# Performance work log

Measured on AMD Instinct MI355X. Metric: run time of the kernel, lower is better.

## Reference

```python
import jax, jax.numpy as jnp
import numpy as np

N = 50000
E = 800000
NEG_SLOPE = 0.2


def gat_layer(x, src, dst, W, al, ar):
    # x: [N, F_in]; W: [F_in, H*D]; al/ar: [H, D]
    H, D = al.shape
    feat = (x @ W).reshape(N, H, D)                      # [N, H, D]
    el = jnp.einsum('nhd,hd->nh', feat, al)              # [N, H]
    er = jnp.einsum('nhd,hd->nh', feat, ar)              # [N, H]
    e = jax.nn.leaky_relu(el[src] + er[dst], NEG_SLOPE)  # [E, H]
    # segment softmax over edges grouped by destination node
    m = jax.ops.segment_max(e, dst, num_segments=N)      # [N, H] (-inf for empty)
    a = jnp.exp(e - m[dst])                              # [E, H]
    s = jax.ops.segment_sum(a, dst, num_segments=N)      # [N, H]
    a = a / jnp.where(s[dst] > 0, s[dst], 1.0)
    # weighted gather-aggregate of messages
    out = jax.ops.segment_sum(a[:, :, None] * feat[src], dst, num_segments=N)
    return out                                           # [N, H, D]


def setup_inputs() -> dict:
    key = jax.random.key(0)
    ks = jax.random.split(key, 9)
    in_size, hid, out_size = 512, 64, 64
    H1, H2 = 4, 4
    return {
        'x':   jax.random.normal(ks[0], (N, in_size), dtype=jnp.float32),
        'src': jax.random.randint(ks[1], (E,), 0, N, dtype=jnp.int32),
        'dst': jax.random.randint(ks[2], (E,), 0, N, dtype=jnp.int32),
        'W1':  jax.random.normal(ks[3], (in_size, H1 * hid), dtype=jnp.float32) * 0.05,
        'al1': jax.random.normal(ks[4], (H1, hid), dtype=jnp.float32) * 0.1,
        'ar1': jax.random.normal(ks[5], (H1, hid), dtype=jnp.float32) * 0.1,
        'W2':  jax.random.normal(ks[6], (H1 * hid, H2 * out_size), dtype=jnp.float32) * 0.05,
        'al2': jax.random.normal(ks[7], (H2, out_size), dtype=jnp.float32) * 0.1,
        'ar2': jax.random.normal(ks[8], (H2, out_size), dtype=jnp.float32) * 0.1,
    }


def reference(x, src, dst, W1, al1, ar1, W2, al2, ar2):
    h = gat_layer(x, src, dst, W1, al1, ar1)   # [N, H1, hid]
    h = jax.nn.elu(h).reshape(N, -1)           # flatten heads -> [N, H1*hid]
    h = gat_layer(h, src, dst, W2, al2, ar2)   # [N, H2, out]
    return h.mean(axis=1)                      # mean over heads -> [N, out]
```

## Files before the change

kernel.cpp:

```cpp
#include <hip/hip_runtime.h>

#define NNODES 50000
#define NEDGES 800000
#define HH 4
#define DD 64
#define FEAT 256
#define NB ((NNODES + 255) / 256)
#define MPAD 50048

typedef __attribute__((ext_vector_type(8))) _Float16 frag16;
typedef __attribute__((ext_vector_type(4))) float frag_cd;
typedef __attribute__((ext_vector_type(4))) _Float16 h4v;
typedef __attribute__((ext_vector_type(8))) _Float16 h8v;

__global__ __launch_bounds__(256) void prep_w_kernel(
    const float* __restrict__ W1, const float* __restrict__ W2,
    _Float16* __restrict__ Bp1, _Float16* __restrict__ Bp2) {
  int idx = blockIdx.x * 256 + threadIdx.x;
  if (idx < 512 * 256) {
    int k = idx >> 8, n = idx & 255;
    Bp1[(size_t)n * 512 + k] = (_Float16)W1[idx];
  } else {
    idx -= 512 * 256;
    int k = idx >> 8, n = idx & 255;
    Bp2[(size_t)n * 256 + k] = (_Float16)W2[idx];
  }
}

template <int AF32>
__global__ __launch_bounds__(512) void mfma_gemm_kernel(
    const void* __restrict__ Av, const _Float16* __restrict__ Bp,
    _Float16* __restrict__ featb, const float* __restrict__ al,
    const float* __restrict__ ar, float* __restrict__ elp,
    float* __restrict__ erp, int M, int K) {
  __shared__ _Float16 As[128 * 64];
  __shared__ _Float16 Bs[256 * 64];
  const int tid = threadIdx.x;
  const int w = tid >> 6, lane = tid & 63;
  const int q = lane >> 4, ln = lane & 15;
  const int rowBase = blockIdx.x * 128;
  const int wm = (w >> 2) * 64;
  const int wn = (w & 3) * 64;

  frag_cd acc[4][4] = {};

  const int i1 = K >> 6;
  const int srow8 = lane >> 3;
  const int scg = ((lane & 7) ^ srow8) * 8;
  const int sw = ln & 7;

  const int ar_ = tid >> 2, aq = tid & 3;
  const int as0 = ((aq * 2) ^ (ar_ & 7)) * 8;
  const int as1 = ((aq * 2 + 1) ^ (ar_ & 7)) * 8;

  for (int it = 0; it < i1; ++it) {
    const int kk = it << 6;
    __syncthreads();
    if constexpr (AF32) {
      const float* __restrict__ x = (const float*)Av;
      float4 v0, v1, v2, v3;
      v0 = v1 = v2 = v3 = make_float4(0.f, 0.f, 0.f, 0.f);
      int xrow = rowBase + ar_;
      if (xrow < M) {
        const float4* xp = (const float4*)(x + (size_t)xrow * 512 + kk + aq * 16);
        v0 = xp[0]; v1 = xp[1]; v2 = xp[2]; v3 = xp[3];
      }
      frag16 f0, f1;
      f0[0] = (_Float16)v0.x; f0[1] = (_Float16)v0.y;
      f0[2] = (_Float16)v0.z; f0[3] = (_Float16)v0.w;
      f0[4] = (_Float16)v1.x; f0[5] = (_Float16)v1.y;
      f0[6] = (_Float16)v1.z; f0[7] = (_Float16)v1.w;
      f1[0] = (_Float16)v2.x; f1[1] = (_Float16)v2.y;
      f1[2] = (_Float16)v2.z; f1[3] = (_Float16)v2.w;
      f1[4] = (_Float16)v3.x; f1[5] = (_Float16)v3.y;
      f1[6] = (_Float16)v3.z; f1[7] = (_Float16)v3.w;
      *(frag16*)&As[ar_ * 64 + as0] = f0;
      *(frag16*)&As[ar_ * 64 + as1] = f1;
    } else {
      const _Float16* __restrict__ Ap = (const _Float16*)Av;
#pragma unroll
      for (int j = 0; j < 2; ++j) {
        int rloc = w * 16 + j * 8 + srow8;
        __builtin_amdgcn_global_load_lds(
            (const __attribute__((address_space(1))) void*)(Ap + (size_t)(rowBase + rloc) * K + kk + scg),
            (__attribute__((address_space(3))) void*)(&As[(w * 16 + j * 8) * 64 + lane * 8]), 16, 0, 0);
      }
    }
#pragma unroll
    for (int j = 0; j < 4; ++j) {
      int rloc = w * 32 + j * 8 + srow8;
      __builtin_amdgcn_global_load_lds(
          (const __attribute__((address_space(1))) void*)(Bp + (size_t)rloc * K + kk + scg),
          (__attribute__((address_space(3))) void*)(&Bs[(w * 32 + j * 8) * 64 + lane * 8]), 16, 0, 0);
    }
    __syncthreads();

#pragma unroll
    for (int ksub = 0; ksub < 2; ++ksub) {
      const int slot = ((ksub * 4 + q) ^ sw) * 8;
      frag16 a[4], b[4];
#pragma unroll
      for (int i = 0; i < 4; ++i)
        a[i] = *(const frag16*)&As[(wm + i * 16 + ln) * 64 + slot];
#pragma unroll
      for (int j = 0; j < 4; ++j)
        b[j] = *(const frag16*)&Bs[(wn + j * 16 + ln) * 64 + slot];
#pragma unroll
      for (int i = 0; i < 4; ++i)
#pragma unroll
        for (int j = 0; j < 4; ++j)
          acc[i][j] = __builtin_amdgcn_mfma_f32_16x16x32_f16(a[i], b[j], acc[i][j], 0, 0, 0);
    }
  }

#pragma unroll
  for (int i = 0; i < 4; ++i) {
    int rowg = rowBase + wm + i * 16 + q * 4;
#pragma unroll
    for (int r = 0; r < 4; ++r) {
      int row = rowg + r;
      if (row < M) {
#pragma unroll
        for (int j = 0; j < 4; ++j) {
          int col = wn + j * 16 + ln;
          featb[(size_t)row * 256 + col] = (_Float16)acc[i][j][r];
        }
      }
    }
  }

  const int h = wn >> 6;
  float alv[4], arv[4];
#pragma unroll
  for (int j = 0; j < 4; ++j) {
    alv[j] = al[h * DD + j * 16 + ln];
    arv[j] = ar[h * DD + j * 16 + ln];
  }
#pragma unroll
  for (int i = 0; i < 4; ++i) {
#pragma unroll
    for (int r = 0; r < 4; ++r) {
      float pl = 0.f, pr = 0.f;
#pragma unroll
      for (int j = 0; j < 4; ++j) {
        pl = fmaf(acc[i][j][r], alv[j], pl);
        pr = fmaf(acc[i][j][r], arv[j], pr);
      }
#pragma unroll
      for (int msk = 1; msk < 16; msk <<= 1) {
        pl += __shfl_xor(pl, msk);
        pr += __shfl_xor(pr, msk);
      }
      int row = rowBase + wm + i * 16 + q * 4 + r;
      if (ln == 0 && row < M) {
        elp[row * HH + h] = pl;
        erp[row * HH + h] = pr;
      }
    }
  }
}

__global__ __launch_bounds__(256) void hist_kernel(const int* __restrict__ dst,
                                                   int* __restrict__ deg) {
  int e = blockIdx.x * 256 + threadIdx.x;
  if (e < NEDGES) atomicAdd(&deg[dst[e]], 1);
}

__global__ __launch_bounds__(256) void scan_block_kernel(const int* __restrict__ deg,
                                                         int* __restrict__ off,
                                                         int* __restrict__ bsum) {
  __shared__ int tmp[256];
  int b = blockIdx.x, t = threadIdx.x;
  int i = b * 256 + t;
  int v = (i < NNODES) ? deg[i] : 0;
  tmp[t] = v;
  __syncthreads();
  for (int s = 1; s < 256; s <<= 1) {
    int add = (t >= s) ? tmp[t - s] : 0;
    __syncthreads();
    tmp[t] += add;
    __syncthreads();
  }
  if (i < NNODES) off[i + 1] = tmp[t];
  if (t == 255) bsum[b] = tmp[255];
}

__global__ __launch_bounds__(256) void scan_top_kernel(int* __restrict__ bsum) {
  __shared__ int tmp[256];
  int t = threadIdx.x;
  int v = (t < NB) ? bsum[t] : 0;
  tmp[t] = v;
  __syncthreads();
  for (int s = 1; s < 256; s <<= 1) {
    int add = (t >= s) ? tmp[t - s] : 0;
    __syncthreads();
    tmp[t] += add;
    __syncthreads();
  }
  if (t < NB) bsum[t] = tmp[t] - v;
}

__global__ __launch_bounds__(256) void scan_add_kernel(int* __restrict__ off,
                                                       const int* __restrict__ bsum,
                                                       int* __restrict__ cursor) {
  int b = blockIdx.x, t = threadIdx.x;
  int i = b * 256 + t;
  if (i < NNODES) {
    int val = off[i + 1] + bsum[b];
    off[i + 1] = val;
    if (i + 1 < NNODES) cursor[i + 1] = val;
  }
  if (i == 0) { off[0] = 0; cursor[0] = 0; }
}

__global__ __launch_bounds__(256) void scatter_kernel(const int* __restrict__ src,
                                                      const int* __restrict__ dst,
                                                      int* __restrict__ cursor,
                                                      int* __restrict__ csr_src) {
  int e = blockIdx.x * 256 + threadIdx.x;
  if (e >= NEDGES) return;
  int d = dst[e];
  int pos = atomicAdd(&cursor[d], 1);
  csr_src[pos] = src[e];
}

template <int LAYER>
__global__ __launch_bounds__(256) void gat_agg_kernel(
    const int* __restrict__ off, const int* __restrict__ csr_src,
    const float* __restrict__ el, const float* __restrict__ er,
    const _Float16* __restrict__ featb, float* __restrict__ outp,
    _Float16* __restrict__ outs) {
  __shared__ float sA[4][HH][68];
  __shared__ int sS[4][64];
  const int w = threadIdx.x >> 6;
  const int lane = threadIdx.x & 63;
  const int n = blockIdx.x * 4 + w;
  const int beg = off[n];
  const int deg = off[n + 1] - beg;

  const int half = lane >> 5;
  const int fl = lane & 31;
  const int fb = fl << 3;
  const int hh = fl >> 3;

  float acc[8] = {0.f, 0.f, 0.f, 0.f, 0.f, 0.f, 0.f, 0.f};

  if (deg > 0 && deg <= 64) {
    const int h1 = lane & 3, j1 = lane >> 2;
    const float erd = er[n * HH + h1];
    float e[4], a[4];
    float m = -INFINITY;
#pragma unroll
    for (int p = 0; p < 4; ++p) {
      int j = j1 + p * 16;
      int s = 0;
      float ev = -INFINITY;
      if (j < deg) {
        s = csr_src[beg + j];
        ev = el[s * HH + h1] + erd;
        ev = ev > 0.f ? ev : 0.2f * ev;
      }
      if (h1 == 0) sS[w][j] = s;
      e[p] = ev;
      m = fmaxf(m, ev);
    }
#pragma unroll
    for (int msk = 4; msk <= 32; msk <<= 1) m = fmaxf(m, __shfl_xor(m, msk));
    float ps = 0.f;
#pragma unroll
    for (int p = 0; p < 4; ++p) {
      a[p] = (j1 + p * 16 < deg) ? __expf(e[p] - m) : 0.f;
      ps += a[p];
    }
#pragma unroll
    for (int msk = 4; msk <= 32; msk <<= 1) ps += __shfl_xor(ps, msk);
    const float sinv = 1.f / ps;
#pragma unroll
    for (int p = 0; p < 4; ++p) {
      int j = j1 + p * 16;
      sA[w][h1][j] = a[p] * sinv;
    }

    const int deg2 = (deg + 1) & ~1;
    int j = 0;
    for (; j + 8 <= deg2; j += 8) {
      int s0 = sS[w][j + half];
      int s1 = sS[w][j + 2 + half];
      int s2 = sS[w][j + 4 + half];
      int s3 = sS[w][j + 6 + half];
      float a0 = sA[w][hh][j + half];
      float a1 = sA[w][hh][j + 2 + half];
      float a2 = sA[w][hh][j + 4 + half];
      float a3 = sA[w][hh][j + 6 + half];
      h8v u0 = *(const h8v*)&featb[(size_t)s0 * FEAT + fb];
      h8v u1 = *(const h8v*)&featb[(size_t)s1 * FEAT + fb];
      h8v u2 = *(const h8v*)&featb[(size_t)s2 * FEAT + fb];
      h8v u3 = *(const h8v*)&featb[(size_t)s3 * FEAT + fb];
#pragma unroll
      for (int c = 0; c < 8; ++c) acc[c] = fmaf(a0, (float)u0[c], acc[c]);
#pragma unroll
      for (int c = 0; c < 8; ++c) acc[c] = fmaf(a1, (float)u1[c], acc[c]);
#pragma unroll
      for (int c = 0; c < 8; ++c) acc[c] = fmaf(a2, (float)u2[c], acc[c]);
#pragma unroll
      for (int c = 0; c < 8; ++c) acc[c] = fmaf(a3, (float)u3[c], acc[c]);
    }
    for (; j < deg2; j += 2) {
      int s0 = sS[w][j + half];
      float a0 = sA[w][hh][j + half];
      h8v u0 = *(const h8v*)&featb[(size_t)s0 * FEAT + fb];
#pragma unroll
      for (int c = 0; c < 8; ++c) acc[c] = fmaf(a0, (float)u0[c], acc[c]);
    }
  } else if (deg > 64) {
    const int h1 = lane & 3, j1 = lane >> 2;
    const float erd = er[n * HH + h1];
    float m = -INFINITY;
    for (int j = j1; j < deg; j += 16) {
      int s = csr_src[beg + j];
      float ev = el[s * HH + h1] + erd;
      ev = ev > 0.f ? ev : 0.2f * ev;
      m = fmaxf(m, ev);
    }
#pragma unroll
    for (int msk = 4; msk <= 32; msk <<= 1) m = fmaxf(m, __shfl_xor(m, msk));
    float ps = 0.f;
    for (int j = j1; j < deg; j += 16) {
      int s = csr_src[beg + j];
      float ev = el[s * HH + h1] + erd;
      ev = ev > 0.f ? ev : 0.2f * ev;
      ps += __expf(ev - m);
    }
#pragma unroll
    for (int msk = 4; msk <= 32; msk <<= 1) ps += __shfl_xor(ps, msk);
    const float m2 = __shfl(m, hh);
    const float psinv2 = 1.f / __shfl(ps, hh);
    const float erd2 = er[n * HH + hh];
    for (int j = half; j < deg; j += 2) {
      int s = csr_src[beg + j];
      float ev = el[s * HH + hh] + erd2;
      ev = ev > 0.f ? ev : 0.2f * ev;
      float a0 = __expf(ev - m2) * psinv2;
      h8v u0 = *(const h8v*)&featb[(size_t)s * FEAT + fb];
#pragma unroll
      for (int c = 0; c < 8; ++c) acc[c] = fmaf(a0, (float)u0[c], acc[c]);
    }
  }

#pragma unroll
  for (int c = 0; c < 8; ++c) acc[c] += __shfl_xor(acc[c], 32);

  if (LAYER == 1) {
    if (half == 0) {
      h8v o;
#pragma unroll
      for (int c = 0; c < 8; ++c) {
        float v = acc[c];
        v = v > 0.f ? v : (__expf(v) - 1.f);
        o[c] = (_Float16)v;
      }
      *(h8v*)&outs[(size_t)n * 256 + fb] = o;
    }
  } else {
#pragma unroll
    for (int c = 0; c < 8; ++c) {
      acc[c] += __shfl_xor(acc[c], 8);
      acc[c] += __shfl_xor(acc[c], 16);
    }
    if (lane < 8) {
      float4 o1 = make_float4(0.25f * acc[0], 0.25f * acc[1],
                              0.25f * acc[2], 0.25f * acc[3]);
      float4 o2 = make_float4(0.25f * acc[4], 0.25f * acc[5],
                              0.25f * acc[6], 0.25f * acc[7]);
      *(float4*)&outp[(size_t)n * DD + (lane << 3)] = o1;
      *(float4*)&outp[(size_t)n * DD + (lane << 3) + 4] = o2;
    }
  }
}

extern "C" void kernel_launch(void* const* d_in, const int* in_sizes, int n_in,
                              void* d_out, int out_size, void* d_ws, size_t ws_size,
                              hipStream_t stream) {
  const float* x   = (const float*)d_in[0];
  const int*   src = (const int*)d_in[1];
  const int*   dst = (const int*)d_in[2];
  const float* W1  = (const float*)d_in[3];
  const float* al1 = (const float*)d_in[4];
  const float* ar1 = (const float*)d_in[5];
  const float* W2  = (const float*)d_in[6];
  const float* al2 = (const float*)d_in[7];
  const float* ar2 = (const float*)d_in[8];
  float* out = (float*)d_out;

  float* ws = (float*)d_ws;
  float* el = ws;
  float* er = el + NNODES * HH;
  int* deg     = (int*)(er + NNODES * HH);
  int* off     = deg + NNODES;
  int* cursor  = off + NNODES + 1;
  int* bsum    = cursor + NNODES;
  int* csr_src = bsum + 256;
  uintptr_t p = ((uintptr_t)(csr_src + NEDGES) + 63) & ~(uintptr_t)63;
  _Float16* featb = (_Float16*)p;
  _Float16* Apr = featb + (size_t)NNODES * 256;
  Apr = (_Float16*)(((uintptr_t)Apr + 63) & ~(uintptr_t)63);
  _Float16* Bpr1 = Apr + (size_t)MPAD * 256;
  _Float16* Bpr2 = Bpr1 + 256 * 512;

  const int edgeBlocks = (NEDGES + 255) / 256;

  hipMemsetAsync(deg, 0, NNODES * sizeof(int), stream);
  hist_kernel<<<edgeBlocks, 256, 0, stream>>>(dst, deg);
  scan_block_kernel<<<NB, 256, 0, stream>>>(deg, off, bsum);
  scan_top_kernel<<<1, 256, 0, stream>>>(bsum);
  scan_add_kernel<<<NB, 256, 0, stream>>>(off, bsum, cursor);
  scatter_kernel<<<edgeBlocks, 256, 0, stream>>>(src, dst, cursor, csr_src);

  prep_w_kernel<<<768, 256, 0, stream>>>(W1, W2, Bpr1, Bpr2);

  mfma_gemm_kernel<1><<<MPAD / 128, 512, 0, stream>>>(x, Bpr1, featb, al1, ar1, el, er, NNODES, 512);
  gat_agg_kernel<1><<<NNODES / 4, 256, 0, stream>>>(off, csr_src, el, er, featb, nullptr, Apr);

  mfma_gemm_kernel<0><<<MPAD / 128, 512, 0, stream>>>(Apr, Bpr2, featb, al2, ar2, el, er, NNODES, 256);
  gat_agg_kernel<2><<<NNODES / 4, 256, 0, stream>>>(off, csr_src, el, er, featb, out, nullptr);
}
```

Baseline: 409.7 us.

## Double-buffer GEMM with smaller M tile, fuse histogram/weight prep, single-block scan

The GEMM tile shrinks from 128 to 64 rows, so twice as many blocks launch, and shared-memory staging becomes double-buffered so the next K slice loads while MFMAs run on the current one. The histogram and weight-transpose kernels merge into one launch. The three-kernel prefix scan becomes a single 1024-thread block that scans 49 elements per thread serially. Together these cut launch count and hide GEMM load latency, at the cost of more B-tile reloads per row and a serial, strided scan pass.

```diff
diff --git a/kernel.cpp b/kernel.cpp
--- a/kernel.cpp
+++ b/kernel.cpp
@@ -5,212 +5,64 @@
 #define HH 4
 #define DD 64
 #define FEAT 256
-#define NB ((NNODES + 255) / 256)
 #define MPAD 50048
+#define EDGEBLOCKS ((NEDGES + 255) / 256)
 
 typedef __attribute__((ext_vector_type(8))) _Float16 frag16;
 typedef __attribute__((ext_vector_type(4))) float frag_cd;
 typedef __attribute__((ext_vector_type(4))) _Float16 h4v;
 typedef __attribute__((ext_vector_type(8))) _Float16 h8v;
 
-__global__ __launch_bounds__(256) void prep_w_kernel(
+__global__ __launch_bounds__(256) void front_kernel(
+    const int* __restrict__ dst, int* __restrict__ deg,
     const float* __restrict__ W1, const float* __restrict__ W2,
     _Float16* __restrict__ Bp1, _Float16* __restrict__ Bp2) {
-  int idx = blockIdx.x * 256 + threadIdx.x;
-  if (idx < 512 * 256) {
-    int k = idx >> 8, n = idx & 255;
-    Bp1[(size_t)n * 512 + k] = (_Float16)W1[idx];
+  int b = blockIdx.x;
+  if (b < EDGEBLOCKS) {
+    int e = b * 256 + threadIdx.x;
+    if (e < NEDGES) atomicAdd(&deg[dst[e]], 1);
   } else {
-    idx -= 512 * 256;
-    int k = idx >> 8, n = idx & 255;
-    Bp2[(size_t)n * 256 + k] = (_Float16)W2[idx];
-  }
-}
-
-template <int AF32>
-__global__ __launch_bounds__(512) void mfma_gemm_kernel(
-    const void* __restrict__ Av, const _Float16* __restrict__ Bp,
-    _Float16* __restrict__ featb, const float* __restrict__ al,
-    const float* __restrict__ ar, float* __restrict__ elp,
-    float* __restrict__ erp, int M, int K) {
-  __shared__ _Float16 As[128 * 64];
-  __shared__ _Float16 Bs[256 * 64];
-  const int tid = threadIdx.x;
-  const int w = tid >> 6, lane = tid & 63;
-  const int q = lane >> 4, ln = lane & 15;
-  const int rowBase = blockIdx.x * 128;
-  const int wm = (w >> 2) * 64;
-  const int wn = (w & 3) * 64;
-
-  frag_cd acc[4][4] = {};
-
-  const int i1 = K >> 6;
-  const int srow8 = lane >> 3;
-  const int scg = ((lane & 7) ^ srow8) * 8;
-  const int sw = ln & 7;
-
-  const int ar_ = tid >> 2, aq = tid & 3;
-  const int as0 = ((aq * 2) ^ (ar_ & 7)) * 8;
-  const int as1 = ((aq * 2 + 1) ^ (ar_ & 7)) * 8;
-
-  for (int it = 0; it < i1; ++it) {
-    const int kk = it << 6;
+    int idx = (b - EDGEBLOCKS) * 256 + threadIdx.x;
+    if (idx < 512 * 256) {
+      int k = idx >> 8, n = idx & 255;
+      Bp1[(size_t)n * 512 + k] = (_Float16)W1[idx];
+    } else {
+      idx -= 512 * 256;
+      int k = idx >> 8, n = idx & 255;
+      Bp2[(size_t)n * 256 + k] = (_Float16)W2[idx];
+    }
+  }
+}
+
+__global__ __launch_bounds__(1024) void scan_kernel(const int* __restrict__ deg,
+                                                    int* __restrict__ off,
+                                                    int* __restrict__ cursor) {
+  __shared__ int part[1024];
+  const int t = threadIdx.x;
+  const int b0 = t * 49;
+  int s = 0;
+  for (int k = 0; k < 49; ++k) {
+    int i = b0 + k;
+    s += (i < NNODES) ? deg[i] : 0;
+  }
+  part[t] = s;
+  __syncthreads();
+  for (int st = 1; st < 1024; st <<= 1) {
+    int add = (t >= st) ? part[t - st] : 0;
     __syncthreads();
-    if constexpr (AF32) {
-      const float* __restrict__ x = (const float*)Av;
-      float4 v0, v1, v2, v3;
-      v0 = v1 = v2 = v3 = make_float4(0.f, 0.f, 0.f, 0.f);
-      int xrow = rowBase + ar_;
-      if (xrow < M) {
-        const float4* xp = (const float4*)(x + (size_t)xrow * 512 + kk + aq * 16);
-        v0 = xp[0]; v1 = xp[1]; v2 = xp[2]; v3 = xp[3];
-      }
-      frag16 f0, f1;
-      f0[0] = (_Float16)v0.x; f0[1] = (_Float16)v0.y;
-      f0[2] = (_Float16)v0.z; f0[3] = (_Float16)v0.w;
-      f0[4] = (_Float16)v1.x; f0[5] = (_Float16)v1.y;
-      f0[6] = (_Float16)v1.z; f0[7] = (_Float16)v1.w;
-      f1[0] = (_Float16)v2.x; f1[1] = (_Float16)v2.y;
-      f1[2] = (_Float16)v2.z; f1[3] = (_Float16)v2.w;
-      f1[4] = (_Float16)v3.x; f1[5] = (_Float16)v3.y;
-      f1[6] = (_Float16)v3.z; f1[7] = (_Float16)v3.w;
-      *(frag16*)&As[ar_ * 64 + as0] = f0;
-      *(frag16*)&As[ar_ * 64 + as1] = f1;
-    } else {
-      const _Float16* __restrict__ Ap = (const _Float16*)Av;
-#pragma unroll
-      for (int j = 0; j < 2; ++j) {
-        int rloc = w * 16 + j * 8 + srow8;
-        __builtin_amdgcn_global_load_lds(
-            (const __attribute__((address_space(1))) void*)(Ap + (size_t)(rowBase + rloc) * K + kk + scg),
-            (__attribute__((address_space(3))) void*)(&As[(w * 16 + j * 8) * 64 + lane * 8]), 16, 0, 0);
-      }
-    }
-#pragma unroll
-    for (int j = 0; j < 4; ++j) {
-      int rloc = w * 32 + j * 8 + srow8;
-      __builtin_amdgcn_global_load_lds(
-          (const __attribute__((address_space(1))) void*)(Bp + (size_t)rloc * K + kk + scg),
-          (__attribute__((address_space(3))) void*)(&Bs[(w * 32 + j * 8) * 64 + lane * 8]), 16, 0, 0);
-    }
+    part[t] += add;
     __syncthreads();
-
-#pragma unroll
-    for (int ksub = 0; ksub < 2; ++ksub) {
-      const int slot = ((ksub * 4 + q) ^ sw) * 8;
-      frag16 a[4], b[4];
-#pragma unroll
-      for (int i = 0; i < 4; ++i)
-        a[i] = *(const frag16*)&As[(wm + i * 16 + ln) * 64 + slot];
-#pragma unroll
-      for (int j = 0; j < 4; ++j)
-        b[j] = *(const frag16*)&Bs[(wn + j * 16 + ln) * 64 + slot];
-#pragma unroll
-      for (int i = 0; i < 4; ++i)
-#pragma unroll
-        for (int j = 0; j < 4; ++j)
-          acc[i][j] = __builtin_amdgcn_mfma_f32_16x16x32_f16(a[i], b[j], acc[i][j], 0, 0, 0);
-    }
-  }
-
-#pragma unroll
-  for (int i = 0; i < 4; ++i) {
-    int rowg = rowBase + wm + i * 16 + q * 4;
-#pragma unroll
-    for (int r = 0; r < 4; ++r) {
-      int row = rowg + r;
-      if (row < M) {
-#pragma unroll
-        for (int j = 0; j < 4; ++j) {
-          int col = wn + j * 16 + ln;
-          featb[(size_t)row * 256 + col] = (_Float16)acc[i][j][r];
-        }
-      }
-    }
-  }
-
-  const int h = wn >> 6;
-  float alv[4], arv[4];
-#pragma unroll
-  for (int j = 0; j < 4; ++j) {
-    alv[j] = al[h * DD + j * 16 + ln];
-    arv[j] = ar[h * DD + j * 16 + ln];
-  }
-#pragma unroll
-  for (int i = 0; i < 4; ++i) {
-#pragma unroll
-    for (int r = 0; r < 4; ++r) {
-      float pl = 0.f, pr = 0.f;
-#pragma unroll
-      for (int j = 0; j < 4; ++j) {
-        pl = fmaf(acc[i][j][r], alv[j], pl);
-        pr = fmaf(acc[i][j][r], arv[j], pr);
-      }
-#pragma unroll
-      for (int msk = 1; msk < 16; msk <<= 1) {
-        pl += __shfl_xor(pl, msk);
-        pr += __shfl_xor(pr, msk);
-      }
-      int row = rowBase + wm + i * 16 + q * 4 + r;
-      if (ln == 0 && row < M) {
-        elp[row * HH + h] = pl;
-        erp[row * HH + h] = pr;
-      }
-    }
-  }
-}
-
-__global__ __launch_bounds__(256) void hist_kernel(const int* __restrict__ dst,
-                                                   int* __restrict__ deg) {
-  int e = blockIdx.x * 256 + threadIdx.x;
-  if (e < NEDGES) atomicAdd(&deg[dst[e]], 1);
-}
-
-__global__ __launch_bounds__(256) void scan_block_kernel(const int* __restrict__ deg,
-                                                         int* __restrict__ off,
-                                                         int* __restrict__ bsum) {
-  __shared__ int tmp[256];
-  int b = blockIdx.x, t = threadIdx.x;
-  int i = b * 256 + t;
-  int v = (i < NNODES) ? deg[i] : 0;
-  tmp[t] = v;
-  __syncthreads();
-  for (int s = 1; s < 256; s <<= 1) {
-    int add = (t >= s) ? tmp[t - s] : 0;
-    __syncthreads();
-    tmp[t] += add;
-    __syncthreads();
-  }
-  if (i < NNODES) off[i + 1] = tmp[t];
-  if (t == 255) bsum[b] = tmp[255];
-}
-
-__global__ __launch_bounds__(256) void scan_top_kernel(int* __restrict__ bsum) {
-  __shared__ int tmp[256];
-  int t = threadIdx.x;
-  int v = (t < NB) ? bsum[t] : 0;
-  tmp[t] = v;
-  __syncthreads();
-  for (int s = 1; s < 256; s <<= 1) {
-    int add = (t >= s) ? tmp[t - s] : 0;
-    __syncthreads();
-    tmp[t] += add;
-    __syncthreads();
-  }
-  if (t < NB) bsum[t] = tmp[t] - v;
-}
-
-__global__ __launch_bounds__(256) void scan_add_kernel(int* __restrict__ off,
-                                                       const int* __restrict__ bsum,
-                                                       int* __restrict__ cursor) {
-  int b = blockIdx.x, t = threadIdx.x;
-  int i = b * 256 + t;
-  if (i < NNODES) {
-    int val = off[i + 1] + bsum[b];
-    off[i + 1] = val;
-    if (i + 1 < NNODES) cursor[i + 1] = val;
-  }
-  if (i == 0) { off[0] = 0; cursor[0] = 0; }
+  }
+  int run = (t == 0) ? 0 : part[t - 1];
+  for (int k = 0; k < 49; ++k) {
+    int i = b0 + k;
+    if (i < NNODES) {
+      off[i] = run;
+      cursor[i] = run;
+      run += deg[i];
+    }
+  }
+  if (t == 1023) off[NNODES] = part[1023];
 }
 
 __global__ __launch_bounds__(256) void scatter_kernel(const int* __restrict__ src,
@@ -222,6 +74,169 @@
   int d = dst[e];
   int pos = atomicAdd(&cursor[d], 1);
   csr_src[pos] = src[e];
+}
+
+template <int AF32>
+__global__ __launch_bounds__(512) void mfma_gemm_kernel(
+    const void* __restrict__ Av, const _Float16* __restrict__ Bp,
+    _Float16* __restrict__ featb, const float* __restrict__ al,
+    const float* __restrict__ ar, float* __restrict__ elp,
+    float* __restrict__ erp, int M, int K) {
+  __shared__ _Float16 As[2][64 * 64];
+  __shared__ _Float16 Bs[2][256 * 64];
+  const int tid = threadIdx.x;
+  const int w = tid >> 6, lane = tid & 63;
+  const int q = lane >> 4, ln = lane & 15;
+  const int rowBase = blockIdx.x * 64;
+  const int wm = (w >> 2) * 32;
+  const int wn = (w & 3) * 64;
+
+  frag_cd acc[2][4] = {};
+
+  const int nt = K >> 6;
+  const int srow8 = lane >> 3;
+  const int scg = ((lane & 7) ^ srow8) * 8;
+  const int sw = ln & 7;
+
+  const int ar_ = tid >> 3, ao = tid & 7;
+  const int aslot = (ao ^ (ar_ & 7)) * 8;
+  const int xrow = rowBase + ar_;
+
+  const float* __restrict__ x = (const float*)Av;
+  const _Float16* __restrict__ Ap = (const _Float16*)Av;
+
+  float4 av0, av1;
+
+  {
+    const int kk = 0;
+    if constexpr (AF32) {
+      av0 = av1 = make_float4(0.f, 0.f, 0.f, 0.f);
+      if (xrow < M) {
+        const float4* xp = (const float4*)(x + (size_t)xrow * 512 + kk + ao * 8);
+        av0 = xp[0]; av1 = xp[1];
+      }
+    } else {
+      __builtin_amdgcn_global_load_lds(
+          (const __attribute__((address_space(1))) void*)(Ap + (size_t)(rowBase + w * 8 + srow8) * K + kk + scg),
+          (__attribute__((address_space(3))) void*)(&As[0][(w * 8) * 64 + lane * 8]), 16, 0, 0);
+    }
+#pragma unroll
+    for (int j = 0; j < 4; ++j) {
+      int rloc = w * 32 + j * 8 + srow8;
+      __builtin_amdgcn_global_load_lds(
+          (const __attribute__((address_space(1))) void*)(Bp + (size_t)rloc * K + kk + scg),
+          (__attribute__((address_space(3))) void*)(&Bs[0][(w * 32 + j * 8) * 64 + lane * 8]), 16, 0, 0);
+    }
+    if constexpr (AF32) {
+      frag16 f;
+      f[0] = (_Float16)av0.x; f[1] = (_Float16)av0.y;
+      f[2] = (_Float16)av0.z; f[3] = (_Float16)av0.w;
+      f[4] = (_Float16)av1.x; f[5] = (_Float16)av1.y;
+      f[6] = (_Float16)av1.z; f[7] = (_Float16)av1.w;
+      *(frag16*)&As[0][ar_ * 64 + aslot] = f;
+    }
+  }
+
+  for (int t = 0; t < nt; ++t) {
+    const int cur = t & 1, nxt = cur ^ 1;
+    __syncthreads();
+
+    if (t + 1 < nt) {
+      const int kk = (t + 1) << 6;
+      if constexpr (AF32) {
+        av0 = av1 = make_float4(0.f, 0.f, 0.f, 0.f);
+        if (xrow < M) {
+          const float4* xp = (const float4*)(x + (size_t)xrow * 512 + kk + ao * 8);
+          av0 = xp[0]; av1 = xp[1];
+        }
+      } else {
+        __builtin_amdgcn_global_load_lds(
+            (const __attribute__((address_space(1))) void*)(Ap + (size_t)(rowBase + w * 8 + srow8) * K + kk + scg),
+            (__attribute__((address_space(3))) void*)(&As[nxt][(w * 8) * 64 + lane * 8]), 16, 0, 0);
+      }
+#pragma unroll
+      for (int j = 0; j < 4; ++j) {
+        int rloc = w * 32 + j * 8 + srow8;
+        __builtin_amdgcn_global_load_lds(
+            (const __attribute__((address_space(1))) void*)(Bp + (size_t)rloc * K + kk + scg),
+            (__attribute__((address_space(3))) void*)(&Bs[nxt][(w * 32 + j * 8) * 64 + lane * 8]), 16, 0, 0);
+      }
+    }
+
+#pragma unroll
+    for (int ksub = 0; ksub < 2; ++ksub) {
+      const int slot = ((ksub * 4 + q) ^ sw) * 8;
+      frag16 a[2], b[4];
+#pragma unroll
+      for (int i = 0; i < 2; ++i)
+        a[i] = *(const frag16*)&As[cur][(wm + i * 16 + ln) * 64 + slot];
+#pragma unroll
+      for (int j = 0; j < 4; ++j)
+        b[j] = *(const frag16*)&Bs[cur][(wn + j * 16 + ln) * 64 + slot];
+#pragma unroll
+      for (int i = 0; i < 2; ++i)
+#pragma unroll
+        for (int j = 0; j < 4; ++j)
+          acc[i][j] = __builtin_amdgcn_mfma_f32_16x16x32_f16(a[i], b[j], acc[i][j], 0, 0, 0);
+    }
+
+    if constexpr (AF32) {
+      if (t + 1 < nt) {
+        frag16 f;
+        f[0] = (_Float16)av0.x; f[1] = (_Float16)av0.y;
+        f[2] = (_Float16)av0.z; f[3] = (_Float16)av0.w;
+        f[4] = (_Float16)av1.x; f[5] = (_Float16)av1.y;
+        f[6] = (_Float16)av1.z; f[7] = (_Float16)av1.w;
+        *(frag16*)&As[nxt][ar_ * 64 + aslot] = f;
+      }
+    }
+  }
+
+#pragma unroll
+  for (int i = 0; i < 2; ++i) {
+    int rowg = rowBase + wm + i * 16 + q * 4;
+#pragma unroll
+    for (int r = 0; r < 4; ++r) {
+      int row = rowg + r;
+      if (row < M) {
+#pragma unroll
+        for (int j = 0; j < 4; ++j) {
+          int col = wn + j * 16 + ln;
+          featb[(size_t)row * 256 + col] = (_Float16)acc[i][j][r];
+        }
+      }
+    }
+  }
+
+  const int h = wn >> 6;
+  float alv[4], arv[4];
+#pragma unroll
+  for (int j = 0; j < 4; ++j) {
+    alv[j] = al[h * DD + j * 16 + ln];
+    arv[j] = ar[h * DD + j * 16 + ln];
+  }
+#pragma unroll
+  for (int i = 0; i < 2; ++i) {
+#pragma unroll
+    for (int r = 0; r < 4; ++r) {
+      float pl = 0.f, pr = 0.f;
+#pragma unroll
+      for (int j = 0; j < 4; ++j) {
+        pl = fmaf(acc[i][j][r], alv[j], pl);
+        pr = fmaf(acc[i][j][r], arv[j], pr);
+      }
+#pragma unroll
+      for (int msk = 1; msk < 16; msk <<= 1) {
+        pl += __shfl_xor(pl, msk);
+        pr += __shfl_xor(pr, msk);
+      }
+      int row = rowBase + wm + i * 16 + q * 4 + r;
+      if (ln == 0 && row < M) {
+        elp[row * HH + h] = pl;
+        erp[row * HH + h] = pr;
+      }
+    }
+  }
 }
 
 template <int LAYER>
@@ -398,8 +413,7 @@
   int* deg     = (int*)(er + NNODES * HH);
   int* off     = deg + NNODES;
   int* cursor  = off + NNODES + 1;
-  int* bsum    = cursor + NNODES;
-  int* csr_src = bsum + 256;
+  int* csr_src = cursor + NNODES;
   uintptr_t p = ((uintptr_t)(csr_src + NEDGES) + 63) & ~(uintptr_t)63;
   _Float16* featb = (_Float16*)p;
   _Float16* Apr = featb + (size_t)NNODES * 256;
@@ -407,20 +421,14 @@
   _Float16* Bpr1 = Apr + (size_t)MPAD * 256;
   _Float16* Bpr2 = Bpr1 + 256 * 512;
 
-  const int edgeBlocks = (NEDGES + 255) / 256;
-
   hipMemsetAsync(deg, 0, NNODES * sizeof(int), stream);
-  hist_kernel<<<edgeBlocks, 256, 0, stream>>>(dst, deg);
-  scan_block_kernel<<<NB, 256, 0, stream>>>(deg, off, bsum);
-  scan_top_kernel<<<1, 256, 0, stream>>>(bsum);
-  scan_add_kernel<<<NB, 256, 0, stream>>>(off, bsum, cursor);
-  scatter_kernel<<<edgeBlocks, 256, 0, stream>>>(src, dst, cursor, csr_src);
-
-  prep_w_kernel<<<768, 256, 0, stream>>>(W1, W2, Bpr1, Bpr2);
-
-  mfma_gemm_kernel<1><<<MPAD / 128, 512, 0, stream>>>(x, Bpr1, featb, al1, ar1, el, er, NNODES, 512);
+  front_kernel<<<EDGEBLOCKS + 768, 256, 0, stream>>>(dst, deg, W1, W2, Bpr1, Bpr2);
+  scan_kernel<<<1, 1024, 0, stream>>>(deg, off, cursor);
+  scatter_kernel<<<EDGEBLOCKS, 256, 0, stream>>>(src, dst, cursor, csr_src);
+
+  mfma_gemm_kernel<1><<<MPAD / 64, 512, 0, stream>>>(x, Bpr1, featb, al1, ar1, el, er, NNODES, 512);
   gat_agg_kernel<1><<<NNODES / 4, 256, 0, stream>>>(off, csr_src, el, er, featb, nullptr, Apr);
 
-  mfma_gemm_kernel<0><<<MPAD / 128, 512, 0, stream>>>(Apr, Bpr2, featb, al2, ar2, el, er, NNODES, 256);
+  mfma_gemm_kernel<0><<<MPAD / 64, 512, 0, stream>>>(Apr, Bpr2, featb, al2, ar2, el, er, NNODES, 256);
   gat_agg_kernel<2><<<NNODES / 4, 256, 0, stream>>>(off, csr_src, el, er, featb, out, nullptr);
 }
```

Result: slower. 526.5 us (+28.5%).
